# Kernel optimization log

Measured on AMD Instinct MI355X. Metric: run time of the kernel, lower is better.

The kernel has to match this reference:

```python
import jax, jax.numpy as jnp
import numpy as np

B, L, D, H = 4, 2048, 1024, 16
DV = D // H


def setup_inputs() -> dict:
    key = jax.random.key(0)
    ks = jax.random.split(key, 11)
    s = 1.0 / np.sqrt(D)
    return {
        "query": jax.random.normal(ks[0], (B, L, D), jnp.float32),
        "key": jax.random.normal(ks[1], (B, L, D), jnp.float32),
        "value": jax.random.normal(ks[2], (B, L, D), jnp.float32),
        "Wq": jax.random.normal(ks[3], (D, D), jnp.float32) * s,
        "bq": jnp.zeros((D,), jnp.float32),
        "Wk": jax.random.normal(ks[4], (D, D), jnp.float32) * s,
        "bk": jnp.zeros((D,), jnp.float32),
        "Wv": jax.random.normal(ks[5], (D, D), jnp.float32) * s,
        "bv": jnp.zeros((D,), jnp.float32),
        "Wc": jax.random.normal(ks[6], (D, D), jnp.float32) * s,
        "bc": jnp.zeros((D,), jnp.float32),
    }


def _split(x):
    # [B, L, D] -> [B, H, L, DV]
    b, l, d = x.shape
    return x.reshape(b, l, H, DV).transpose(0, 2, 1, 3)


def reference(query, key, value, Wq, bq, Wk, bk, Wv, bv, Wc, bc):
    # Linear projections (torch Linear: x @ W.T + b)
    hq = _split(query @ Wq.T + bq)
    hk = _split(key @ Wk.T + bk)
    hv = _split(value @ Wv.T + bv)
    scale = 1.0 / jnp.sqrt(jnp.float32(DV))
    scores = jnp.einsum("bhqd,bhkd->bhqk", hq, hk) * scale  # [B,H,L,L]
    p = jax.nn.softmax(scores, axis=-1)
    out = jnp.einsum("bhqk,bhkd->bhqd", p, hv)  # [B,H,L,DV]
    out = out.transpose(0, 2, 1, 3).reshape(out.shape[0], out.shape[2], D)
    return out @ Wc.T + bc
```

## Files before the change

kernel.cpp:

```cpp
#include <hip/hip_runtime.h>

#define DI __device__ __forceinline__

typedef __attribute__((ext_vector_type(8))) short bf16x8;
typedef __attribute__((ext_vector_type(4))) float f32x4;
typedef __attribute__((ext_vector_type(16))) float f32x16;
typedef __attribute__((ext_vector_type(4))) unsigned u32x4;
typedef __attribute__((ext_vector_type(2))) unsigned u32x2;

static constexpr int B_ = 4, L_ = 2048, D_ = 1024, H_ = 16, DV_ = 64;
static constexpr int M_ = B_ * L_;
static constexpr float SCALE_LOG2 = 0.18033688011112042f;

DI short f2b(float f) {
  union { float f; unsigned u; } v; v.f = f;
  unsigned r = v.u + 0x7FFFu + ((v.u >> 16) & 1u);
  return (short)(r >> 16);
}

DI float b2f(short s) {
  union { unsigned u; float f; } v;
  v.u = ((unsigned)(unsigned short)s) << 16;
  return v.f;
}

DI unsigned cvtpk(float lo, float hi) {
  unsigned r;
  asm("v_cvt_pk_bf16_f32 %0, %1, %2" : "=v"(r) : "v"(lo), "v"(hi));
  return r;
}

DI void gl_lds16(const void* g, void* l) {
  __builtin_amdgcn_global_load_lds(
      (const __attribute__((address_space(1))) unsigned int*)g,
      (__attribute__((address_space(3))) unsigned int*)l, 16, 0, 0);
}

#define MFMA16(a, b, c) __builtin_amdgcn_mfma_f32_16x16x32_bf16((a), (b), (c), 0, 0, 0)
#define MFMA32(a, b, c) __builtin_amdgcn_mfma_f32_32x32x16_bf16((a), (b), (c), 0, 0, 0)

__global__ __launch_bounds__(256) void cvt_kernel(const float* __restrict__ src,
                                                  short* __restrict__ dst, int n) {
  int i0 = (blockIdx.x * 256 + threadIdx.x) * 8;
  int stride = gridDim.x * 256 * 8;
  for (int i = i0; i < n; i += stride) {
    float4 a = *(const float4*)(src + i);
    float4 b = *(const float4*)(src + i + 4);
    bf16x8 o;
    o[0] = f2b(a.x); o[1] = f2b(a.y); o[2] = f2b(a.z); o[3] = f2b(a.w);
    o[4] = f2b(b.x); o[5] = f2b(b.y); o[6] = f2b(b.z); o[7] = f2b(b.w);
    *(bf16x8*)(dst + i) = o;
  }
}

template <int OUTF32>
__global__ __launch_bounds__(256) void gemm_bt(const short* __restrict__ A,
                                               const short* __restrict__ Wt,
                                               const float* __restrict__ bias,
                                               float* __restrict__ outf,
                                               short* __restrict__ outb) {
  constexpr int K = 1024, N = 1024;
  __shared__ short As[128 * 32];
  __shared__ short Bs[128 * 32];
  const int tid = threadIdx.x;
  const int w = tid >> 6, lane = tid & 63;
  const int c = lane & 15, g = lane >> 4;
  const int bid = (blockIdx.x & 7) * 64 + (blockIdx.x >> 3);
  const int bn = bid & 7, bm = bid >> 3;
  const int wr = w >> 1, wc = w & 1;

  f32x4 acc[4][4] = {};

  for (int kt = 0; kt < K / 32; ++kt) {
    __syncthreads();
#pragma unroll
    for (int ia = 0; ia < 2; ++ia) {
      int slot = ia * 256 + tid;
      int row = slot >> 2, ch = slot & 3;
      gl_lds16(A + ((size_t)(bm * 128 + row) * K + kt * 32 + ch * 8),
               &As[(ia * 256 + w * 64) * 8]);
      gl_lds16(Wt + ((size_t)(bn * 128 + row) * K + kt * 32 + ch * 8),
               &Bs[(ia * 256 + w * 64) * 8]);
    }
    __syncthreads();
    bf16x8 af[4], bf[4];
#pragma unroll
    for (int mi = 0; mi < 4; ++mi)
      af[mi] = *(const bf16x8*)&As[(wr * 64 + mi * 16 + c) * 32 + g * 8];
#pragma unroll
    for (int ni = 0; ni < 4; ++ni)
      bf[ni] = *(const bf16x8*)&Bs[(wc * 64 + ni * 16 + c) * 32 + g * 8];
#pragma unroll
    for (int mi = 0; mi < 4; ++mi)
#pragma unroll
      for (int ni = 0; ni < 4; ++ni)
        acc[mi][ni] = MFMA16(af[mi], bf[ni], acc[mi][ni]);
  }

  float bv[4];
#pragma unroll
  for (int ni = 0; ni < 4; ++ni) bv[ni] = bias[bn * 128 + wc * 64 + ni * 16 + c];
#pragma unroll
  for (int mi = 0; mi < 4; ++mi)
#pragma unroll
    for (int ni = 0; ni < 4; ++ni)
#pragma unroll
      for (int j = 0; j < 4; ++j) {
        int row = bm * 128 + wr * 64 + mi * 16 + g * 4 + j;
        int col = bn * 128 + wc * 64 + ni * 16 + c;
        float v = acc[mi][ni][j] + bv[ni];
        if (OUTF32)
          outf[(size_t)row * N + col] = v;
        else
          outb[(size_t)row * N + col] = f2b(v);
      }
}

__global__ __launch_bounds__(256) void transpose_kernel(const short* __restrict__ Hv,
                                                        short* __restrict__ Hvt) {
  __shared__ short T[64 * 72];
  int bid = blockIdx.x;
  const int lt = bid & 31;
  const int h = (bid >> 5) & 15;
  const int b = bid >> 9;
  const int l0 = lt * 64;
  const int tid = threadIdx.x;
#pragma unroll
  for (int it = 0; it < 2; ++it) {
    int slot = it * 256 + tid;
    int r = slot >> 3, ch = slot & 7;
    bf16x8 v = *(const bf16x8*)&Hv[(size_t)(b * L_ + l0 + r) * D_ + h * DV_ + ch * 8];
    *(bf16x8*)&T[r * 72 + ch * 8] = v;
  }
  __syncthreads();
#pragma unroll
  for (int it = 0; it < 2; ++it) {
    int slot = it * 256 + tid;
    int dv = slot >> 3, ch = slot & 7;
    bf16x8 o;
#pragma unroll
    for (int i = 0; i < 8; ++i) o[i] = T[(ch * 8 + i) * 72 + dv];
    *(bf16x8*)&Hvt[(size_t)((b * H_ + h) * DV_ + dv) * L_ + l0 + ch * 8] = o;
  }
}

__global__ __launch_bounds__(512, 2) void attn_kernel(const short* __restrict__ Hq,
                                                      const short* __restrict__ Hk,
                                                      const short* __restrict__ Hvt,
                                                      short* __restrict__ Aout) {
  __shared__ __align__(16) short lds[33280];
  const int tid = threadIdx.x;
  const int w = tid >> 6, lane = tid & 63;
  const int c31 = lane & 31, g1 = lane >> 5;
  const int sw = (blockIdx.x & 7) * 64 + (blockIdx.x >> 3);
  const int qb = sw & 7;
  const int h = (sw >> 3) & 15;
  const int b = sw >> 7;
  const int q0 = qb * 256;

  const short* qptr = Hq + (size_t)(b * L_ + q0 + w * 32 + c31) * D_ + h * 64 + g1 * 8;
  bf16x8 qf[4];
#pragma unroll
  for (int ks = 0; ks < 4; ++ks) {
    bf16x8 raw = *(const bf16x8*)(qptr + ks * 16);
    u32x4 pk;
#pragma unroll
    for (int i = 0; i < 4; ++i)
      pk[i] = cvtpk(b2f(raw[2 * i]) * SCALE_LOG2, b2f(raw[2 * i + 1]) * SCALE_LOG2);
    qf[ks] = __builtin_bit_cast(bf16x8, pk);
  }

  f32x16 O0 = {}, O1 = {};
  float ls = 0.f;
  unsigned* Pw = (unsigned*)(lds + 16384) + w * 1056;

  auto stage = [&](int buf, int kv0) {
    short* Kb = lds + buf * 8192;
    short* Vb = Kb + 4096;
    int row = tid >> 3;
    int ch = (tid & 7) ^ (row & 7);
    gl_lds16(Hk + (size_t)(b * L_ + kv0 + row) * D_ + h * 64 + ch * 8, Kb + w * 512);
    gl_lds16(Hvt + (size_t)((b * H_ + h) * DV_ + row) * L_ + kv0 + ch * 8, Vb + w * 512);
  };

  stage(0, 0);
  int cur = 0;
  for (int t = 0; t < L_ / 64; ++t) {
    __syncthreads();
    if (t + 1 < L_ / 64) stage(cur ^ 1, (t + 1) * 64);
    const short* Kb = lds + cur * 8192;
    const short* Vb = Kb + 4096;

    f32x16 s0 = {}, s1 = {};
#pragma unroll
    for (int ks = 0; ks < 4; ++ks) {
      int cp = (((2 * ks + g1) ^ (c31 & 7)) * 8);
      bf16x8 k0 = *(const bf16x8*)(Kb + c31 * 64 + cp);
      bf16x8 k1 = *(const bf16x8*)(Kb + (32 + c31) * 64 + cp);
      s0 = MFMA32(k0, qf[ks], s0);
      s1 = MFMA32(k1, qf[ks], s1);
    }

    float rs = 0.f;
#pragma unroll
    for (int i = 0; i < 8; ++i) {
      float a0 = __builtin_amdgcn_exp2f(s0[2 * i]);
      float a1 = __builtin_amdgcn_exp2f(s0[2 * i + 1]);
      float c0 = __builtin_amdgcn_exp2f(s1[2 * i]);
      float c1 = __builtin_amdgcn_exp2f(s1[2 * i + 1]);
      rs += (a0 + a1) + (c0 + c1);
      int kr = (i & 1) + 4 * (i >> 1) + 2 * g1;
      Pw[kr * 33 + c31] = cvtpk(a0, a1);
      Pw[(16 + kr) * 33 + c31] = cvtpk(c0, c1);
    }
    ls += rs + __shfl_xor(rs, 32);

#pragma unroll
    for (int ks2 = 0; ks2 < 4; ++ks2) {
      const unsigned* pb = Pw + (ks2 * 8 + g1 * 4) * 33 + c31;
      u32x4 pk;
      pk[0] = pb[0];
      pk[1] = pb[33];
      pk[2] = pb[66];
      pk[3] = pb[99];
      bf16x8 pf = __builtin_bit_cast(bf16x8, pk);
      int cp = (((2 * ks2 + g1) ^ (c31 & 7)) * 8);
      bf16x8 vf0 = *(const bf16x8*)(Vb + c31 * 64 + cp);
      bf16x8 vf1 = *(const bf16x8*)(Vb + (32 + c31) * 64 + cp);
      O0 = MFMA32(vf0, pf, O0);
      O1 = MFMA32(vf1, pf, O1);
    }
    cur ^= 1;
  }

  float inv = 1.0f / ls;
  __syncthreads();
  short* Os = lds;
#pragma unroll
  for (int dt = 0; dt < 2; ++dt) {
#pragma unroll
    for (int rq = 0; rq < 4; ++rq) {
      float e0 = (dt ? O1[4 * rq] : O0[4 * rq]) * inv;
      float e1 = (dt ? O1[4 * rq + 1] : O0[4 * rq + 1]) * inv;
      float e2 = (dt ? O1[4 * rq + 2] : O0[4 * rq + 2]) * inv;
      float e3 = (dt ? O1[4 * rq + 3] : O0[4 * rq + 3]) * inv;
      u32x2 pr;
      pr[0] = cvtpk(e0, e1);
      pr[1] = cvtpk(e2, e3);
      int q = w * 32 + c31;
      int dv = dt * 32 + 8 * rq + 4 * g1;
      *(u32x2*)&Os[q * 72 + dv] = pr;
    }
  }
  __syncthreads();
  const int r = tid >> 1, hf = tid & 1;
  const size_t obase = (size_t)(b * L_ + q0 + r) * D_ + h * 64 + hf * 32;
#pragma unroll
  for (int cc = 0; cc < 4; ++cc) {
    bf16x8 vv = *(const bf16x8*)&Os[r * 72 + hf * 32 + cc * 8];
    *(bf16x8*)&Aout[obase + cc * 8] = vv;
  }
}

extern "C" void kernel_launch(void* const* d_in, const int* in_sizes, int n_in,
                              void* d_out, int out_size, void* d_ws, size_t ws_size,
                              hipStream_t stream) {
  (void)in_sizes; (void)n_in; (void)out_size; (void)ws_size;
  const float* q = (const float*)d_in[0];
  const float* k = (const float*)d_in[1];
  const float* v = (const float*)d_in[2];
  const float* Wq = (const float*)d_in[3];
  const float* bq = (const float*)d_in[4];
  const float* Wk = (const float*)d_in[5];
  const float* bk = (const float*)d_in[6];
  const float* Wv = (const float*)d_in[7];
  const float* bv = (const float*)d_in[8];
  const float* Wc = (const float*)d_in[9];
  const float* bc = (const float*)d_in[10];
  float* out = (float*)d_out;

  short* ws = (short*)d_ws;
  const size_t SZ = (size_t)M_ * D_;
  const size_t WSZ = (size_t)D_ * D_;
  short* conv = ws;
  short* wqb = ws + SZ;
  short* wkb = wqb + WSZ;
  short* wvb = wkb + WSZ;
  short* wcb = wvb + WSZ;
  short* hq = wcb + WSZ;
  short* hk = hq + SZ;
  short* hv = hk + SZ;
  short* hvt = conv;
  short* aout = hv;

  cvt_kernel<<<512, 256, 0, stream>>>(Wq, wqb, (int)WSZ);
  cvt_kernel<<<512, 256, 0, stream>>>(Wk, wkb, (int)WSZ);
  cvt_kernel<<<512, 256, 0, stream>>>(Wv, wvb, (int)WSZ);
  cvt_kernel<<<512, 256, 0, stream>>>(Wc, wcb, (int)WSZ);

  cvt_kernel<<<1024, 256, 0, stream>>>(q, conv, (int)SZ);
  gemm_bt<0><<<512, 256, 0, stream>>>(conv, wqb, bq, nullptr, hq);
  cvt_kernel<<<1024, 256, 0, stream>>>(k, conv, (int)SZ);
  gemm_bt<0><<<512, 256, 0, stream>>>(conv, wkb, bk, nullptr, hk);
  cvt_kernel<<<1024, 256, 0, stream>>>(v, conv, (int)SZ);
  gemm_bt<0><<<512, 256, 0, stream>>>(conv, wvb, bv, nullptr, hv);

  transpose_kernel<<<2048, 256, 0, stream>>>(hv, hvt);

  attn_kernel<<<512, 512, 0, stream>>>(hq, hk, hvt, aout);

  gemm_bt<1><<<512, 256, 0, stream>>>(aout, wcb, bc, out, nullptr);
}
```

Measured before the change: 237.0 us.

## Fuse fp32-to-bf16 input conversion into batched QKV projection GEMM

Replaces the separate per-input conversion kernels and three projection GEMMs with a single launch that streams fp32 activations straight into shared memory and converts them to bf16 in-register before the MFMAs. The four weight conversions are merged into one launch with packed bf16 conversion. s_setprio is also raised around the MFMA blocks in the attention kernel. This removes the bf16 activation round trip through memory and several launches, at the cost of twice the A-tile shared-memory traffic and extra conversion work inside the GEMM loop.

```diff
diff --git a/kernel.cpp b/kernel.cpp
--- a/kernel.cpp
+++ b/kernel.cpp
@@ -39,18 +39,111 @@
 #define MFMA16(a, b, c) __builtin_amdgcn_mfma_f32_16x16x32_bf16((a), (b), (c), 0, 0, 0)
 #define MFMA32(a, b, c) __builtin_amdgcn_mfma_f32_32x32x16_bf16((a), (b), (c), 0, 0, 0)
 
-__global__ __launch_bounds__(256) void cvt_kernel(const float* __restrict__ src,
-                                                  short* __restrict__ dst, int n) {
+__global__ __launch_bounds__(256) void cvtw_kernel(const float* __restrict__ W0,
+                                                   const float* __restrict__ W1,
+                                                   const float* __restrict__ W2,
+                                                   const float* __restrict__ W3,
+                                                   short* __restrict__ dst) {
+  const int p = blockIdx.y;
+  const float* s = p == 0 ? W0 : p == 1 ? W1 : p == 2 ? W2 : W3;
+  short* d = dst + (size_t)p * 1048576;
   int i0 = (blockIdx.x * 256 + threadIdx.x) * 8;
   int stride = gridDim.x * 256 * 8;
-  for (int i = i0; i < n; i += stride) {
-    float4 a = *(const float4*)(src + i);
-    float4 b = *(const float4*)(src + i + 4);
-    bf16x8 o;
-    o[0] = f2b(a.x); o[1] = f2b(a.y); o[2] = f2b(a.z); o[3] = f2b(a.w);
-    o[4] = f2b(b.x); o[5] = f2b(b.y); o[6] = f2b(b.z); o[7] = f2b(b.w);
-    *(bf16x8*)(dst + i) = o;
-  }
+  for (int i = i0; i < 1048576; i += stride) {
+    float4 a = *(const float4*)(s + i);
+    float4 b = *(const float4*)(s + i + 4);
+    u32x4 o;
+    o[0] = cvtpk(a.x, a.y);
+    o[1] = cvtpk(a.z, a.w);
+    o[2] = cvtpk(b.x, b.y);
+    o[3] = cvtpk(b.z, b.w);
+    *(u32x4*)(d + i) = o;
+  }
+}
+
+__global__ __launch_bounds__(256) void gemm_qkvf(const float* __restrict__ Xq,
+                                                 const float* __restrict__ Xk,
+                                                 const float* __restrict__ Xv,
+                                                 const short* __restrict__ Wall,
+                                                 const float* __restrict__ bq,
+                                                 const float* __restrict__ bk,
+                                                 const float* __restrict__ bv,
+                                                 short* __restrict__ Hq,
+                                                 short* __restrict__ Hk,
+                                                 short* __restrict__ Hv) {
+  constexpr int K = 1024, N = 1024;
+  __shared__ float Asf[128 * 32];
+  __shared__ short Bs[128 * 32];
+  const int p = blockIdx.y;
+  const float* A = p == 0 ? Xq : p == 1 ? Xk : Xv;
+  const short* Wt = Wall + (size_t)p * 1048576;
+  const float* bias = p == 0 ? bq : p == 1 ? bk : bv;
+  short* outb = p == 0 ? Hq : p == 1 ? Hk : Hv;
+
+  const int tid = threadIdx.x;
+  const int w = tid >> 6, lane = tid & 63;
+  const int c = lane & 15, g = lane >> 4;
+  const int bid = (blockIdx.x & 7) * 64 + (blockIdx.x >> 3);
+  const int bn = bid & 7, bm = bid >> 3;
+  const int wr = w >> 1, wc = w & 1;
+
+  f32x4 acc[4][4] = {};
+
+  for (int kt = 0; kt < K / 32; ++kt) {
+    __syncthreads();
+#pragma unroll
+    for (int it = 0; it < 4; ++it) {
+      int slot = it * 256 + tid;
+      int row = slot >> 3, ch = (slot & 7) ^ (row & 7);
+      gl_lds16(A + ((size_t)(bm * 128 + row) * K + kt * 32 + ch * 4),
+               &Asf[(it * 256 + w * 64) * 4]);
+    }
+#pragma unroll
+    for (int ia = 0; ia < 2; ++ia) {
+      int slot = ia * 256 + tid;
+      int row = slot >> 2, ch = slot & 3;
+      gl_lds16(Wt + ((size_t)(bn * 128 + row) * K + kt * 32 + ch * 8),
+               &Bs[(ia * 256 + w * 64) * 8]);
+    }
+    __syncthreads();
+    bf16x8 af[4], bf[4];
+#pragma unroll
+    for (int mi = 0; mi < 4; ++mi) {
+      int r = wr * 64 + mi * 16 + c;
+      int c0 = (((2 * g) ^ (r & 7)) * 4);
+      int c1 = (((2 * g + 1) ^ (r & 7)) * 4);
+      float4 lo = *(const float4*)&Asf[r * 32 + c0];
+      float4 hi = *(const float4*)&Asf[r * 32 + c1];
+      u32x4 pk;
+      pk[0] = cvtpk(lo.x, lo.y);
+      pk[1] = cvtpk(lo.z, lo.w);
+      pk[2] = cvtpk(hi.x, hi.y);
+      pk[3] = cvtpk(hi.z, hi.w);
+      af[mi] = __builtin_bit_cast(bf16x8, pk);
+    }
+#pragma unroll
+    for (int ni = 0; ni < 4; ++ni)
+      bf[ni] = *(const bf16x8*)&Bs[(wc * 64 + ni * 16 + c) * 32 + g * 8];
+#pragma unroll
+    for (int mi = 0; mi < 4; ++mi)
+#pragma unroll
+      for (int ni = 0; ni < 4; ++ni)
+        acc[mi][ni] = MFMA16(af[mi], bf[ni], acc[mi][ni]);
+  }
+
+  float bvv[4];
+#pragma unroll
+  for (int ni = 0; ni < 4; ++ni) bvv[ni] = bias[bn * 128 + wc * 64 + ni * 16 + c];
+#pragma unroll
+  for (int mi = 0; mi < 4; ++mi)
+#pragma unroll
+    for (int ni = 0; ni < 4; ++ni)
+#pragma unroll
+      for (int j = 0; j < 4; ++j) {
+        int row = bm * 128 + wr * 64 + mi * 16 + g * 4 + j;
+        int col = bn * 128 + wc * 64 + ni * 16 + c;
+        outb[(size_t)row * N + col] = f2b(acc[mi][ni][j] + bvv[ni]);
+      }
 }
 
 template <int OUTF32>
@@ -192,6 +285,7 @@
     const short* Vb = Kb + 4096;
 
     f32x16 s0 = {}, s1 = {};
+    __builtin_amdgcn_s_setprio(1);
 #pragma unroll
     for (int ks = 0; ks < 4; ++ks) {
       int cp = (((2 * ks + g1) ^ (c31 & 7)) * 8);
@@ -200,6 +294,7 @@
       s0 = MFMA32(k0, qf[ks], s0);
       s1 = MFMA32(k1, qf[ks], s1);
     }
+    __builtin_amdgcn_s_setprio(0);
 
     float rs = 0.f;
 #pragma unroll
@@ -215,6 +310,7 @@
     }
     ls += rs + __shfl_xor(rs, 32);
 
+    __builtin_amdgcn_s_setprio(1);
 #pragma unroll
     for (int ks2 = 0; ks2 < 4; ++ks2) {
       const unsigned* pb = Pw + (ks2 * 8 + g1 * 4) * 33 + c31;
@@ -230,6 +326,7 @@
       O0 = MFMA32(vf0, pf, O0);
       O1 = MFMA32(vf1, pf, O1);
     }
+    __builtin_amdgcn_s_setprio(0);
     cur ^= 1;
   }
 
@@ -282,28 +379,19 @@
   short* ws = (short*)d_ws;
   const size_t SZ = (size_t)M_ * D_;
   const size_t WSZ = (size_t)D_ * D_;
-  short* conv = ws;
-  short* wqb = ws + SZ;
-  short* wkb = wqb + WSZ;
-  short* wvb = wkb + WSZ;
-  short* wcb = wvb + WSZ;
-  short* hq = wcb + WSZ;
+  short* wqb = ws;
+  short* wcb = ws + 3 * WSZ;
+  short* hq = ws + 4 * WSZ;
   short* hk = hq + SZ;
   short* hv = hk + SZ;
-  short* hvt = conv;
+  short* hvt = hv + SZ;
   short* aout = hv;
 
-  cvt_kernel<<<512, 256, 0, stream>>>(Wq, wqb, (int)WSZ);
-  cvt_kernel<<<512, 256, 0, stream>>>(Wk, wkb, (int)WSZ);
-  cvt_kernel<<<512, 256, 0, stream>>>(Wv, wvb, (int)WSZ);
-  cvt_kernel<<<512, 256, 0, stream>>>(Wc, wcb, (int)WSZ);
-
-  cvt_kernel<<<1024, 256, 0, stream>>>(q, conv, (int)SZ);
-  gemm_bt<0><<<512, 256, 0, stream>>>(conv, wqb, bq, nullptr, hq);
-  cvt_kernel<<<1024, 256, 0, stream>>>(k, conv, (int)SZ);
-  gemm_bt<0><<<512, 256, 0, stream>>>(conv, wkb, bk, nullptr, hk);
-  cvt_kernel<<<1024, 256, 0, stream>>>(v, conv, (int)SZ);
-  gemm_bt<0><<<512, 256, 0, stream>>>(conv, wvb, bv, nullptr, hv);
+  dim3 gw(128, 4);
+  cvtw_kernel<<<gw, 256, 0, stream>>>(Wq, Wk, Wv, Wc, wqb);
+
+  dim3 gq(512, 3);
+  gemm_qkvf<<<gq, 256, 0, stream>>>(q, k, v, wqb, bq, bk, bv, hq, hk, hv);
 
   transpose_kernel<<<2048, 256, 0, stream>>>(hv, hvt);
 
```

Result: faster. 205.8 us (-13.2%).
